# Performance work log

Hardware: AMD Instinct MI355X
Metric: run time of the kernel (lower is better)

Reference implementation:

```python
import jax, jax.numpy as jnp
import numpy as np

D_MODEL = 1024
N_HEADS = 16
D_K = D_MODEL // N_HEADS


def setup_inputs() -> dict:
    key = jax.random.key(0)
    ks = jax.random.split(key, 9)
    s = 1.0 / np.sqrt(D_MODEL)
    def lin(kw, kb):
        W = jax.random.uniform(kw, (D_MODEL, D_MODEL), jnp.float32, -s, s)
        b = jax.random.uniform(kb, (D_MODEL,), jnp.float32, -s, s)
        return W, b
    wq, bq = lin(ks[0], ks[1])
    wk, bk = lin(ks[2], ks[3])
    wv, bv = lin(ks[4], ks[5])
    wo, bo = lin(ks[6], ks[7])
    x = jax.random.normal(ks[8], (2, 2048, D_MODEL), jnp.float32)
    return {"x": x, "wq": wq, "bq": bq, "wk": wk, "bk": bk,
            "wv": wv, "bv": bv, "wo": wo, "bo": bo}


def reference(x, wq, bq, wk, bk, wv, bv, wo, bo):
    B, S, D = x.shape
    scale = 1.0 / np.sqrt(D_K)
    # projections (torch Linear: y = x W^T + b); W stored as [in,out] here
    q = x @ wq + bq
    k = x @ wk + bk
    v = x @ wv + bv
    # [B, H, S, d_k]
    q = q.reshape(B, S, N_HEADS, D_K).transpose(0, 2, 1, 3)
    k = k.reshape(B, S, N_HEADS, D_K).transpose(0, 2, 1, 3)
    v = v.reshape(B, S, N_HEADS, D_K).transpose(0, 2, 1, 3)
    scores = jnp.einsum('bhqd,bhkd->bhqk', q, k) * scale
    attn = jax.nn.softmax(scores, axis=-1)
    out = jnp.einsum('bhqk,bhkd->bhqd', attn, v)
    out = out.transpose(0, 2, 1, 3).reshape(B, S, D)
    return out @ wo + bo
```

## Files before the change

### kernel.cpp

```cpp
#include <hip/hip_runtime.h>
#include <hip/hip_bf16.h>
#include <math.h>

typedef __bf16 bf16x8 __attribute__((ext_vector_type(8)));
typedef unsigned short u16x8 __attribute__((ext_vector_type(8)));
typedef unsigned short u16x4 __attribute__((ext_vector_type(4)));
typedef float f32x4 __attribute__((ext_vector_type(4)));
typedef unsigned short u16;

__device__ __forceinline__ u16 f2bf(float f) {
    unsigned int x = __float_as_uint(f);
    x += 0x7fffu + ((x >> 16) & 1u);
    return (u16)(x >> 16);
}
__device__ __forceinline__ void glds16(const void* g, void* l) {
    __builtin_amdgcn_global_load_lds(
        (const __attribute__((address_space(1))) void*)g,
        (__attribute__((address_space(3))) void*)l, 16, 0, 0);
}

__global__ __launch_bounds__(256) void prep(const float* __restrict__ W0, const float* __restrict__ W1,
                                            const float* __restrict__ W2, const float* __restrict__ W3,
                                            const float* __restrict__ X,
                                            u16* __restrict__ Wt, u16* __restrict__ Xb) {
    int z = blockIdx.z;
    if (z >= 4) {
        int row = (z - 4) * 1024 + blockIdx.y * 32 + blockIdx.x;
        const float* src = X + (size_t)row * 1024 + threadIdx.x * 4;
        f32x4 v = *(const f32x4*)src;
        u16x4 o; o[0] = f2bf(v[0]); o[1] = f2bf(v[1]); o[2] = f2bf(v[2]); o[3] = f2bf(v[3]);
        *(u16x4*)&Xb[(size_t)row * 1024 + threadIdx.x * 4] = o;
        return;
    }
    __shared__ float T[32][33];
    const float* W = (z == 0) ? W0 : ((z == 1) ? W1 : ((z == 2) ? W2 : W3));
    u16* dst = Wt + (size_t)z * 1024 * 1024;
    int k0 = blockIdx.y * 32, n0 = blockIdx.x * 32;
    int x = threadIdx.x & 31, y0 = threadIdx.x >> 5;
#pragma unroll
    for (int i = 0; i < 4; i++) {
        int y = y0 + i * 8;
        T[y][x] = W[(size_t)(k0 + y) * 1024 + n0 + x];
    }
    __syncthreads();
#pragma unroll
    for (int i = 0; i < 4; i++) {
        int y = y0 + i * 8;
        dst[(size_t)(n0 + y) * 1024 + k0 + x] = f2bf(T[x][y]);
    }
}

template <bool OF32, bool VSPLIT>
__global__ __launch_bounds__(256) void gemm(
    const u16* __restrict__ Bt,
    const float* __restrict__ b0, const float* __restrict__ b1, const float* __restrict__ b2,
    const u16* __restrict__ A, void* __restrict__ Cptr, u16* __restrict__ Vt, int Ntot)
{
    __shared__ __align__(16) u16 As[128 * 32];
    __shared__ __align__(16) u16 Bs[128 * 32];
    int tid = threadIdx.x;
    int lane = tid & 63, l15 = lane & 15, quad = lane >> 4;
    int wid = tid >> 6, wm = wid >> 1, wn = wid & 1;
    int m0 = blockIdx.y * 128, n0 = blockIdx.x * 128;
    int sel = n0 >> 10;
    const float* bias = (sel == 0) ? b0 : ((sel == 1) ? b1 : b2);

    f32x4 acc[4][4];
#pragma unroll
    for (int i = 0; i < 4; i++)
#pragma unroll
        for (int j = 0; j < 4; j++) { f32x4 z = {0.f, 0.f, 0.f, 0.f}; acc[i][j] = z; }

    int rr = lane >> 2;
    int cc = (lane & 3) ^ ((rr >> 1) & 3);
    const u16* abase = A  + (size_t)m0 * 1024;
    const u16* bbase = Bt + (size_t)n0 * 1024;
    int fsw = (l15 >> 1) & 3;

    for (int k0 = 0; k0 < 1024; k0 += 32) {
#pragma unroll
        for (int inst = 0; inst < 2; inst++) {
            int r0 = wid * 32 + inst * 16;
            glds16(&abase[(size_t)(r0 + rr) * 1024 + k0 + cc * 8], &As[r0 * 32]);
            glds16(&bbase[(size_t)(r0 + rr) * 1024 + k0 + cc * 8], &Bs[r0 * 32]);
        }
        __syncthreads();
        bf16x8 af[4], bf[4];
#pragma unroll
        for (int mt = 0; mt < 4; mt++)
            af[mt] = *(const bf16x8*)&As[(wm * 64 + mt * 16 + l15) * 32 + ((quad ^ fsw) * 8)];
#pragma unroll
        for (int nt = 0; nt < 4; nt++)
            bf[nt] = *(const bf16x8*)&Bs[(wn * 64 + nt * 16 + l15) * 32 + ((quad ^ fsw) * 8)];
#pragma unroll
        for (int mt = 0; mt < 4; mt++)
#pragma unroll
            for (int nt = 0; nt < 4; nt++)
                acc[mt][nt] = __builtin_amdgcn_mfma_f32_16x16x32_bf16(af[mt], bf[nt], acc[mt][nt], 0, 0, 0);
        __syncthreads();
    }
    if (VSPLIT && sel == 2) {
        int b = m0 >> 11;
#pragma unroll
        for (int mt = 0; mt < 4; mt++) {
            int gr = m0 + wm * 64 + mt * 16 + quad * 4;
            int s = gr & 2047;
#pragma unroll
            for (int nt = 0; nt < 4; nt++) {
                int gcl = (n0 & 1023) + wn * 64 + nt * 16 + l15;
                float bb = bias[gcl];
                u16x4 pk;
#pragma unroll
                for (int r = 0; r < 4; r++) pk[r] = f2bf(acc[mt][nt][r] + bb);
                *(u16x4*)&Vt[(size_t)((b * 16 + (gcl >> 6)) * 64 + (gcl & 63)) * 2048 + s] = pk;
            }
        }
        return;
    }
#pragma unroll
    for (int mt = 0; mt < 4; mt++) {
        int gr = m0 + wm * 64 + mt * 16 + quad * 4;
#pragma unroll
        for (int nt = 0; nt < 4; nt++) {
            int gc = n0 + wn * 64 + nt * 16 + l15;
            float bb = bias[gc & 1023];
#pragma unroll
            for (int r = 0; r < 4; r++) {
                float v = acc[mt][nt][r] + bb;
                if (OF32) ((float*)Cptr)[(size_t)(gr + r) * Ntot + gc] = v;
                else      ((u16*)Cptr)[(size_t)(gr + r) * Ntot + gc] = f2bf(v);
            }
        }
    }
}

__global__ __launch_bounds__(256) void attn(const u16* __restrict__ QKV,
                                            const u16* __restrict__ Vt,
                                            u16* __restrict__ O)
{
    __shared__ __align__(16) u16 Ks[64 * 64];
    __shared__ __align__(16) u16 Vs[64 * 64];
    __shared__ __align__(16) u16 Ps[4][16 * 72];
    const int S = 2048, DQ = 3072;
    int tid = threadIdx.x, wid = tid >> 6, lane = tid & 63;
    int l15 = lane & 15, quad = lane >> 4;
    int qt = blockIdx.x, h = blockIdx.y, b = blockIdx.z;
    const u16* base = QKV + (size_t)b * S * DQ + h * 64;
    const u16* Kb = base + 1024;
    const u16* Vtb = Vt + (size_t)((b * 16 + h) * 64) * 2048;
    int q0 = qt * 64 + wid * 16;

    bf16x8 qf0 = *(const bf16x8*)&base[(size_t)(q0 + l15) * DQ + quad * 8];
    bf16x8 qf1 = *(const bf16x8*)&base[(size_t)(q0 + l15) * DQ + 32 + quad * 8];

    f32x4 oacc[4];
#pragma unroll
    for (int i = 0; i < 4; i++) { f32x4 z = {0.f, 0.f, 0.f, 0.f}; oacc[i] = z; }
    float psum[4] = {0.f, 0.f, 0.f, 0.f};
    const float ls = 0.125f * 1.44269504088896f;

    int rr = lane >> 3;
    int cc = (lane & 7) ^ rr;
    int fs7 = l15 & 7;

    for (int kv0 = 0; kv0 < S; kv0 += 64) {
#pragma unroll
        for (int inst = 0; inst < 2; inst++) {
            int r0 = wid * 16 + inst * 8;
            glds16(&Kb[(size_t)(kv0 + r0 + rr) * DQ + cc * 8], &Ks[r0 * 64]);
            glds16(&Vtb[(size_t)(r0 + rr) * 2048 + kv0 + cc * 8], &Vs[r0 * 64]);
        }
        __syncthreads();

        f32x4 sa[4];
#pragma unroll
        for (int t = 0; t < 4; t++) { f32x4 z = {0.f, 0.f, 0.f, 0.f}; sa[t] = z; }
#pragma unroll
        for (int t = 0; t < 4; t++) {
            bf16x8 kfa = *(const bf16x8*)&Ks[(t * 16 + l15) * 64 + ((quad ^ fs7) * 8)];
            bf16x8 kfb = *(const bf16x8*)&Ks[(t * 16 + l15) * 64 + (((quad + 4) ^ fs7) * 8)];
            sa[t] = __builtin_amdgcn_mfma_f32_16x16x32_bf16(qf0, kfa, sa[t], 0, 0, 0);
            sa[t] = __builtin_amdgcn_mfma_f32_16x16x32_bf16(qf1, kfb, sa[t], 0, 0, 0);
        }
        u16* Pw = Ps[wid];
#pragma unroll
        for (int t = 0; t < 4; t++)
#pragma unroll
            for (int r = 0; r < 4; r++) {
                float p = __builtin_amdgcn_exp2f(sa[t][r] * ls);
                psum[r] += p;
                Pw[(quad * 4 + r) * 72 + t * 16 + l15] = f2bf(p);
            }
        __asm__ __volatile__("" ::: "memory");
        bf16x8 pf0 = *(const bf16x8*)&Pw[l15 * 72 + quad * 8];
        bf16x8 pf1 = *(const bf16x8*)&Pw[l15 * 72 + 32 + quad * 8];
#pragma unroll
        for (int dt = 0; dt < 4; dt++) {
            bf16x8 vfa = *(const bf16x8*)&Vs[(dt * 16 + l15) * 64 + ((quad ^ fs7) * 8)];
            bf16x8 vfb = *(const bf16x8*)&Vs[(dt * 16 + l15) * 64 + (((quad + 4) ^ fs7) * 8)];
            oacc[dt] = __builtin_amdgcn_mfma_f32_16x16x32_bf16(pf0, vfa, oacc[dt], 0, 0, 0);
            oacc[dt] = __builtin_amdgcn_mfma_f32_16x16x32_bf16(pf1, vfb, oacc[dt], 0, 0, 0);
        }
        __syncthreads();
    }
#pragma unroll
    for (int r = 0; r < 4; r++) {
        float s = psum[r];
        s += __shfl_xor(s, 1);
        s += __shfl_xor(s, 2);
        s += __shfl_xor(s, 4);
        s += __shfl_xor(s, 8);
        float inv = 1.0f / s;
        size_t row = (size_t)(b * S + q0 + quad * 4 + r);
#pragma unroll
        for (int dt = 0; dt < 4; dt++)
            O[row * 1024 + h * 64 + dt * 16 + l15] = f2bf(oacc[dt][r] * inv);
    }
}

extern "C" void kernel_launch(void* const* d_in, const int* in_sizes, int n_in,
                              void* d_out, int out_size, void* d_ws, size_t ws_size,
                              hipStream_t stream) {
    const float* x  = (const float*)d_in[0];
    const float* wq = (const float*)d_in[1];
    const float* bq = (const float*)d_in[2];
    const float* wk = (const float*)d_in[3];
    const float* bk = (const float*)d_in[4];
    const float* wv = (const float*)d_in[5];
    const float* bv = (const float*)d_in[6];
    const float* wo = (const float*)d_in[7];
    const float* bo = (const float*)d_in[8];
    float* out = (float*)d_out;

    u16* qkv  = (u16*)d_ws;
    u16* obuf = qkv  + (size_t)4096 * 3072;
    u16* vt   = obuf + (size_t)4096 * 1024;
    u16* wt   = vt   + (size_t)2048 * 2048;
    u16* xb   = wt   + (size_t)4 * 1024 * 1024;

    dim3 tb(256);
    prep<<<dim3(32, 32, 8), tb, 0, stream>>>(wq, wk, wv, wo, x, wt, xb);
    gemm<false, true><<<dim3(24, 32), tb, 0, stream>>>(wt, bq, bk, bv, xb, qkv, vt, 3072);
    attn<<<dim3(32, 16, 2), tb, 0, stream>>>(qkv, vt, obuf);
    gemm<true, false><<<dim3(8, 32), tb, 0, stream>>>(wt + (size_t)3 * 1024 * 1024,
                                                      bo, bo, bo, obuf, out, (u16*)nullptr, 1024);
}
```

Measured before the change: 220.6 us.

## Widen GEMM K-tile, give attention waves two Q subtiles, fold softmax scale into projections

The GEMM K step doubles to 64 with an 8-way XOR swizzle, which halves the barrier count per output tile. The attention kernel now runs 2 waves of 128 threads, each owning 32 query rows, so every K/V fragment loaded from LDS feeds two MFMAs. The softmax scale (0.125 for Q, log2e for K) is folded into the projection epilogue, removing a multiply per score. It also vectorizes the weight-transpose store and switches to the native bf16 conversion. In exchange it adds register pressure, and the pre-scaled bf16 Q/K introduce extra rounding.

```diff
diff --git a/kernel.cpp b/kernel.cpp
--- a/kernel.cpp
+++ b/kernel.cpp
@@ -9,9 +9,8 @@
 typedef unsigned short u16;
 
 __device__ __forceinline__ u16 f2bf(float f) {
-    unsigned int x = __float_as_uint(f);
-    x += 0x7fffu + ((x >> 16) & 1u);
-    return (u16)(x >> 16);
+    __bf16 h = (__bf16)f;
+    return *(u16*)&h;
 }
 __device__ __forceinline__ void glds16(const void* g, void* l) {
     __builtin_amdgcn_global_load_lds(
@@ -43,11 +42,11 @@
         T[y][x] = W[(size_t)(k0 + y) * 1024 + n0 + x];
     }
     __syncthreads();
-#pragma unroll
-    for (int i = 0; i < 4; i++) {
-        int y = y0 + i * 8;
-        dst[(size_t)(n0 + y) * 1024 + k0 + x] = f2bf(T[x][y]);
-    }
+    int nl = threadIdx.x >> 3, kq = threadIdx.x & 7;
+    u16x4 o;
+#pragma unroll
+    for (int j = 0; j < 4; j++) o[j] = f2bf(T[kq * 4 + j][nl]);
+    *(u16x4*)&dst[(size_t)(n0 + nl) * 1024 + k0 + kq * 4] = o;
 }
 
 template <bool OF32, bool VSPLIT>
@@ -56,8 +55,8 @@
     const float* __restrict__ b0, const float* __restrict__ b1, const float* __restrict__ b2,
     const u16* __restrict__ A, void* __restrict__ Cptr, u16* __restrict__ Vt, int Ntot)
 {
-    __shared__ __align__(16) u16 As[128 * 32];
-    __shared__ __align__(16) u16 Bs[128 * 32];
+    __shared__ __align__(16) u16 As[128 * 64];
+    __shared__ __align__(16) u16 Bs[128 * 64];
     int tid = threadIdx.x;
     int lane = tid & 63, l15 = lane & 15, quad = lane >> 4;
     int wid = tid >> 6, wm = wid >> 1, wn = wid & 1;
@@ -71,34 +70,40 @@
 #pragma unroll
         for (int j = 0; j < 4; j++) { f32x4 z = {0.f, 0.f, 0.f, 0.f}; acc[i][j] = z; }
 
-    int rr = lane >> 2;
-    int cc = (lane & 3) ^ ((rr >> 1) & 3);
+    int rr = lane >> 3;
+    int cc = (lane & 7) ^ rr;
+    int fs7 = l15 & 7;
     const u16* abase = A  + (size_t)m0 * 1024;
     const u16* bbase = Bt + (size_t)n0 * 1024;
-    int fsw = (l15 >> 1) & 3;
-
-    for (int k0 = 0; k0 < 1024; k0 += 32) {
-#pragma unroll
-        for (int inst = 0; inst < 2; inst++) {
-            int r0 = wid * 32 + inst * 16;
-            glds16(&abase[(size_t)(r0 + rr) * 1024 + k0 + cc * 8], &As[r0 * 32]);
-            glds16(&bbase[(size_t)(r0 + rr) * 1024 + k0 + cc * 8], &Bs[r0 * 32]);
-        }
-        __syncthreads();
-        bf16x8 af[4], bf[4];
-#pragma unroll
-        for (int mt = 0; mt < 4; mt++)
-            af[mt] = *(const bf16x8*)&As[(wm * 64 + mt * 16 + l15) * 32 + ((quad ^ fsw) * 8)];
-#pragma unroll
-        for (int nt = 0; nt < 4; nt++)
-            bf[nt] = *(const bf16x8*)&Bs[(wn * 64 + nt * 16 + l15) * 32 + ((quad ^ fsw) * 8)];
-#pragma unroll
-        for (int mt = 0; mt < 4; mt++)
+
+    for (int k0 = 0; k0 < 1024; k0 += 64) {
+#pragma unroll
+        for (int inst = 0; inst < 4; inst++) {
+            int r0 = wid * 32 + inst * 8;
+            glds16(&abase[(size_t)(r0 + rr) * 1024 + k0 + cc * 8], &As[r0 * 64]);
+            glds16(&bbase[(size_t)(r0 + rr) * 1024 + k0 + cc * 8], &Bs[r0 * 64]);
+        }
+        __syncthreads();
+#pragma unroll
+        for (int h = 0; h < 2; h++) {
+            int kc = quad + 4 * h;
+            bf16x8 af[4], bf[4];
+#pragma unroll
+            for (int mt = 0; mt < 4; mt++)
+                af[mt] = *(const bf16x8*)&As[(wm * 64 + mt * 16 + l15) * 64 + ((kc ^ fs7) * 8)];
 #pragma unroll
             for (int nt = 0; nt < 4; nt++)
-                acc[mt][nt] = __builtin_amdgcn_mfma_f32_16x16x32_bf16(af[mt], bf[nt], acc[mt][nt], 0, 0, 0);
-        __syncthreads();
-    }
+                bf[nt] = *(const bf16x8*)&Bs[(wn * 64 + nt * 16 + l15) * 64 + ((kc ^ fs7) * 8)];
+#pragma unroll
+            for (int mt = 0; mt < 4; mt++)
+#pragma unroll
+                for (int nt = 0; nt < 4; nt++)
+                    acc[mt][nt] = __builtin_amdgcn_mfma_f32_16x16x32_bf16(af[mt], bf[nt], acc[mt][nt], 0, 0, 0);
+        }
+        __syncthreads();
+    }
+    float scl = 1.0f;
+    if (VSPLIT) scl = (sel == 0) ? 0.125f : ((sel == 1) ? 1.44269504088896f : 1.0f);
     if (VSPLIT && sel == 2) {
         int b = m0 >> 11;
 #pragma unroll
@@ -126,7 +131,7 @@
             float bb = bias[gc & 1023];
 #pragma unroll
             for (int r = 0; r < 4; r++) {
-                float v = acc[mt][nt][r] + bb;
+                float v = (acc[mt][nt][r] + bb) * scl;
                 if (OF32) ((float*)Cptr)[(size_t)(gr + r) * Ntot + gc] = v;
                 else      ((u16*)Cptr)[(size_t)(gr + r) * Ntot + gc] = f2bf(v);
             }
@@ -134,13 +139,13 @@
     }
 }
 
-__global__ __launch_bounds__(256) void attn(const u16* __restrict__ QKV,
+__global__ __launch_bounds__(128) void attn(const u16* __restrict__ QKV,
                                             const u16* __restrict__ Vt,
                                             u16* __restrict__ O)
 {
     __shared__ __align__(16) u16 Ks[64 * 64];
     __shared__ __align__(16) u16 Vs[64 * 64];
-    __shared__ __align__(16) u16 Ps[4][16 * 72];
+    __shared__ __align__(16) u16 Ps[2][32 * 72];
     const int S = 2048, DQ = 3072;
     int tid = threadIdx.x, wid = tid >> 6, lane = tid & 63;
     int l15 = lane & 15, quad = lane >> 4;
@@ -148,16 +153,21 @@
     const u16* base = QKV + (size_t)b * S * DQ + h * 64;
     const u16* Kb = base + 1024;
     const u16* Vtb = Vt + (size_t)((b * 16 + h) * 64) * 2048;
-    int q0 = qt * 64 + wid * 16;
-
-    bf16x8 qf0 = *(const bf16x8*)&base[(size_t)(q0 + l15) * DQ + quad * 8];
-    bf16x8 qf1 = *(const bf16x8*)&base[(size_t)(q0 + l15) * DQ + 32 + quad * 8];
-
-    f32x4 oacc[4];
-#pragma unroll
-    for (int i = 0; i < 4; i++) { f32x4 z = {0.f, 0.f, 0.f, 0.f}; oacc[i] = z; }
-    float psum[4] = {0.f, 0.f, 0.f, 0.f};
-    const float ls = 0.125f * 1.44269504088896f;
+    int q0 = qt * 64 + wid * 32;
+
+    bf16x8 qf[2][2];
+#pragma unroll
+    for (int sub = 0; sub < 2; sub++) {
+        qf[sub][0] = *(const bf16x8*)&base[(size_t)(q0 + sub * 16 + l15) * DQ + quad * 8];
+        qf[sub][1] = *(const bf16x8*)&base[(size_t)(q0 + sub * 16 + l15) * DQ + 32 + quad * 8];
+    }
+
+    f32x4 oacc[2][4];
+#pragma unroll
+    for (int s = 0; s < 2; s++)
+#pragma unroll
+        for (int i = 0; i < 4; i++) { f32x4 z = {0.f, 0.f, 0.f, 0.f}; oacc[s][i] = z; }
+    float psum[2][4] = {{0.f, 0.f, 0.f, 0.f}, {0.f, 0.f, 0.f, 0.f}};
 
     int rr = lane >> 3;
     int cc = (lane & 7) ^ rr;
@@ -165,57 +175,73 @@
 
     for (int kv0 = 0; kv0 < S; kv0 += 64) {
 #pragma unroll
-        for (int inst = 0; inst < 2; inst++) {
-            int r0 = wid * 16 + inst * 8;
+        for (int inst = 0; inst < 4; inst++) {
+            int r0 = wid * 32 + inst * 8;
             glds16(&Kb[(size_t)(kv0 + r0 + rr) * DQ + cc * 8], &Ks[r0 * 64]);
             glds16(&Vtb[(size_t)(r0 + rr) * 2048 + kv0 + cc * 8], &Vs[r0 * 64]);
         }
         __syncthreads();
 
-        f32x4 sa[4];
-#pragma unroll
-        for (int t = 0; t < 4; t++) { f32x4 z = {0.f, 0.f, 0.f, 0.f}; sa[t] = z; }
+        f32x4 sa[2][4];
+#pragma unroll
+        for (int s = 0; s < 2; s++)
+#pragma unroll
+            for (int t = 0; t < 4; t++) { f32x4 z = {0.f, 0.f, 0.f, 0.f}; sa[s][t] = z; }
 #pragma unroll
         for (int t = 0; t < 4; t++) {
             bf16x8 kfa = *(const bf16x8*)&Ks[(t * 16 + l15) * 64 + ((quad ^ fs7) * 8)];
             bf16x8 kfb = *(const bf16x8*)&Ks[(t * 16 + l15) * 64 + (((quad + 4) ^ fs7) * 8)];
-            sa[t] = __builtin_amdgcn_mfma_f32_16x16x32_bf16(qf0, kfa, sa[t], 0, 0, 0);
-            sa[t] = __builtin_amdgcn_mfma_f32_16x16x32_bf16(qf1, kfb, sa[t], 0, 0, 0);
+#pragma unroll
+            for (int sub = 0; sub < 2; sub++) {
+                sa[sub][t] = __builtin_amdgcn_mfma_f32_16x16x32_bf16(qf[sub][0], kfa, sa[sub][t], 0, 0, 0);
+                sa[sub][t] = __builtin_amdgcn_mfma_f32_16x16x32_bf16(qf[sub][1], kfb, sa[sub][t], 0, 0, 0);
+            }
         }
         u16* Pw = Ps[wid];
 #pragma unroll
-        for (int t = 0; t < 4; t++)
-#pragma unroll
-            for (int r = 0; r < 4; r++) {
-                float p = __builtin_amdgcn_exp2f(sa[t][r] * ls);
-                psum[r] += p;
-                Pw[(quad * 4 + r) * 72 + t * 16 + l15] = f2bf(p);
-            }
+        for (int sub = 0; sub < 2; sub++)
+#pragma unroll
+            for (int t = 0; t < 4; t++)
+#pragma unroll
+                for (int r = 0; r < 4; r++) {
+                    float p = __builtin_amdgcn_exp2f(sa[sub][t][r]);
+                    psum[sub][r] += p;
+                    Pw[(sub * 16 + quad * 4 + r) * 72 + t * 16 + l15] = f2bf(p);
+                }
         __asm__ __volatile__("" ::: "memory");
-        bf16x8 pf0 = *(const bf16x8*)&Pw[l15 * 72 + quad * 8];
-        bf16x8 pf1 = *(const bf16x8*)&Pw[l15 * 72 + 32 + quad * 8];
+        bf16x8 pf[2][2];
+#pragma unroll
+        for (int sub = 0; sub < 2; sub++) {
+            pf[sub][0] = *(const bf16x8*)&Pw[(sub * 16 + l15) * 72 + quad * 8];
+            pf[sub][1] = *(const bf16x8*)&Pw[(sub * 16 + l15) * 72 + 32 + quad * 8];
+        }
 #pragma unroll
         for (int dt = 0; dt < 4; dt++) {
             bf16x8 vfa = *(const bf16x8*)&Vs[(dt * 16 + l15) * 64 + ((quad ^ fs7) * 8)];
             bf16x8 vfb = *(const bf16x8*)&Vs[(dt * 16 + l15) * 64 + (((quad + 4) ^ fs7) * 8)];
-            oacc[dt] = __builtin_amdgcn_mfma_f32_16x16x32_bf16(pf0, vfa, oacc[dt], 0, 0, 0);
-            oacc[dt] = __builtin_amdgcn_mfma_f32_16x16x32_bf16(pf1, vfb, oacc[dt], 0, 0, 0);
-        }
-        __syncthreads();
-    }
-#pragma unroll
-    for (int r = 0; r < 4; r++) {
-        float s = psum[r];
-        s += __shfl_xor(s, 1);
-        s += __shfl_xor(s, 2);
-        s += __shfl_xor(s, 4);
-        s += __shfl_xor(s, 8);
-        float inv = 1.0f / s;
-        size_t row = (size_t)(b * S + q0 + quad * 4 + r);
-#pragma unroll
-        for (int dt = 0; dt < 4; dt++)
-            O[row * 1024 + h * 64 + dt * 16 + l15] = f2bf(oacc[dt][r] * inv);
-    }
+#pragma unroll
+            for (int sub = 0; sub < 2; sub++) {
+                oacc[sub][dt] = __builtin_amdgcn_mfma_f32_16x16x32_bf16(pf[sub][0], vfa, oacc[sub][dt], 0, 0, 0);
+                oacc[sub][dt] = __builtin_amdgcn_mfma_f32_16x16x32_bf16(pf[sub][1], vfb, oacc[sub][dt], 0, 0, 0);
+            }
+        }
+        __syncthreads();
+    }
+#pragma unroll
+    for (int sub = 0; sub < 2; sub++)
+#pragma unroll
+        for (int r = 0; r < 4; r++) {
+            float s = psum[sub][r];
+            s += __shfl_xor(s, 1);
+            s += __shfl_xor(s, 2);
+            s += __shfl_xor(s, 4);
+            s += __shfl_xor(s, 8);
+            float inv = 1.0f / s;
+            size_t row = (size_t)(b * S + q0 + sub * 16 + quad * 4 + r);
+#pragma unroll
+            for (int dt = 0; dt < 4; dt++)
+                O[row * 1024 + h * 64 + dt * 16 + l15] = f2bf(oacc[sub][dt][r] * inv);
+        }
 }
 
 extern "C" void kernel_launch(void* const* d_in, const int* in_sizes, int n_in,
@@ -238,10 +264,9 @@
     u16* wt   = vt   + (size_t)2048 * 2048;
     u16* xb   = wt   + (size_t)4 * 1024 * 1024;
 
-    dim3 tb(256);
-    prep<<<dim3(32, 32, 8), tb, 0, stream>>>(wq, wk, wv, wo, x, wt, xb);
-    gemm<false, true><<<dim3(24, 32), tb, 0, stream>>>(wt, bq, bk, bv, xb, qkv, vt, 3072);
-    attn<<<dim3(32, 16, 2), tb, 0, stream>>>(qkv, vt, obuf);
-    gemm<true, false><<<dim3(8, 32), tb, 0, stream>>>(wt + (size_t)3 * 1024 * 1024,
-                                                      bo, bo, bo, obuf, out, (u16*)nullptr, 1024);
-}
+    prep<<<dim3(32, 32, 8), dim3(256), 0, stream>>>(wq, wk, wv, wo, x, wt, xb);
+    gemm<false, true><<<dim3(24, 32), dim3(256), 0, stream>>>(wt, bq, bk, bv, xb, qkv, vt, 3072);
+    attn<<<dim3(32, 16, 2), dim3(128), 0, stream>>>(qkv, vt, obuf);
+    gemm<true, false><<<dim3(8, 32), dim3(256), 0, stream>>>(wt + (size_t)3 * 1024 * 1024,
+                                                             bo, bo, bo, obuf, out, (u16*)nullptr, 1024);
+}
```

Result: no change. 225.0 us (+2.0%).
